# Optimization experiments

Hardware: AMD Instinct MI355X
Metric: run time of the kernel (lower is better)

## Reference

```python
import jax, jax.numpy as jnp
import numpy as np

EMBED_DIM = 1024
NUM_HEADS = 16
DIM_HEAD = EMBED_DIM // NUM_HEADS


def setup_inputs() -> dict:
    key = jax.random.key(0)
    ks = jax.random.split(key, 9)
    s = 1.0 / np.sqrt(EMBED_DIM)
    x = jax.random.normal(ks[0], (2, 2048, EMBED_DIM), dtype=jnp.float32)
    Wq = jax.random.uniform(ks[1], (EMBED_DIM, EMBED_DIM), jnp.float32, -s, s)
    bq = jax.random.uniform(ks[2], (EMBED_DIM,), jnp.float32, -s, s)
    Wk = jax.random.uniform(ks[3], (EMBED_DIM, EMBED_DIM), jnp.float32, -s, s)
    bk = jax.random.uniform(ks[4], (EMBED_DIM,), jnp.float32, -s, s)
    Wv = jax.random.uniform(ks[5], (EMBED_DIM, EMBED_DIM), jnp.float32, -s, s)
    bv = jax.random.uniform(ks[6], (EMBED_DIM,), jnp.float32, -s, s)
    Wo = jax.random.uniform(ks[7], (EMBED_DIM, EMBED_DIM), jnp.float32, -s, s)
    bo = jax.random.uniform(ks[8], (EMBED_DIM,), jnp.float32, -s, s)
    return {"x": x, "Wq": Wq, "bq": bq, "Wk": Wk, "bk": bk,
            "Wv": Wv, "bv": bv, "Wo": Wo, "bo": bo}


def reference(x, Wq, bq, Wk, bk, Wv, bv, Wo, bo):
    B, S, _ = x.shape
    # Linear layers (torch nn.Linear: x @ W.T + b), reshape to heads
    Q = (x @ Wq.T + bq).reshape(B, S, NUM_HEADS, DIM_HEAD)
    K = (x @ Wk.T + bk).reshape(B, S, NUM_HEADS, DIM_HEAD)
    V = (x @ Wv.T + bv).reshape(B, S, NUM_HEADS, DIM_HEAD)
    scores = jnp.einsum('bqhd,bkhd->bhqk', Q, K) / np.sqrt(DIM_HEAD)
    attn = jax.nn.softmax(scores, axis=-1)
    context = jnp.einsum('bhqk,bkhd->bqhd', attn, V).reshape(B, S, EMBED_DIM)
    return context @ Wo.T + bo
```

## Files before the change

### kernel.cpp

```cpp
#include <hip/hip_runtime.h>
#include <hip/hip_bf16.h>

#define SEQ   2048
#define EMB   1024
#define NHEAD 16
#define DHEAD 64
#define BATCH 2
#define MTOT  (BATCH*SEQ)
#define QT    64
#define KT    64

typedef __attribute__((ext_vector_type(8))) short s8v;
typedef __attribute__((ext_vector_type(4))) short s4v;
typedef __attribute__((ext_vector_type(4))) float f4v;

__device__ __forceinline__ short f2b(float f) {
    union { float fl; unsigned u; } v; v.fl = f;
    unsigned u = v.u;
    u = (u + 0x7fffu + ((u >> 16) & 1u)) >> 16;
    return (short)u;
}
__device__ __forceinline__ unsigned pk2(float a, float b) {
    union { __hip_bfloat162 h; unsigned u; } c;
    c.h = __float22bfloat162_rn(float2{a, b});
    return c.u;
}

#if __has_builtin(__builtin_amdgcn_exp2f)
__device__ __forceinline__ float exp2_fast(float x) { return __builtin_amdgcn_exp2f(x); }
#else
__device__ __forceinline__ float exp2_fast(float x) { return exp2f(x); }
#endif

__device__ __forceinline__ void pl32swap(unsigned &a, unsigned &b) {
    asm("v_permlane32_swap_b32 %0, %1" : "+v"(a), "+v"(b));
}
__device__ __forceinline__ void pl16swap(unsigned &a, unsigned &b) {
    asm("v_permlane16_swap_b32 %0, %1" : "+v"(a), "+v"(b));
}

__device__ __forceinline__ void bar_lds() {
    asm volatile("s_waitcnt lgkmcnt(0)\n\ts_barrier" ::: "memory");
}

__device__ __forceinline__ void gl_lds16(const short* g, short* l) {
    __builtin_amdgcn_global_load_lds(
        (const __attribute__((address_space(1))) void*)g,
        (__attribute__((address_space(3))) void*)l, 16, 0, 0);
}

__global__ __launch_bounds__(256)
void cvt_swz(const float* __restrict__ s0, const float* __restrict__ s1,
             const float* __restrict__ s2, const float* __restrict__ s3,
             const float* __restrict__ s4,
             short* __restrict__ d0, short* __restrict__ d1,
             short* __restrict__ d2, short* __restrict__ d3,
             short* __restrict__ d4)
{
    const int seg = blockIdx.y;
    const float* s = seg == 0 ? s0 : seg == 1 ? s1 : seg == 2 ? s2 : seg == 3 ? s3 : s4;
    short*       d = seg == 0 ? d0 : seg == 1 ? d1 : seg == 2 ? d2 : seg == 3 ? d3 : d4;
    const int nchunk = (seg == 0 ? MTOT * EMB : EMB * EMB) / 8;
    const int stride = gridDim.x * 256;
    for (int i = blockIdx.x * 256 + threadIdx.x; i < nchunk; i += stride) {
        const int row = i >> 7;
        const int c   = i & 127;
        const float4 v0 = *(const float4*)(s + (size_t)i * 8);
        const float4 v1 = *(const float4*)(s + (size_t)i * 8 + 4);
        s8v o;
        o[0] = f2b(v0.x); o[1] = f2b(v0.y); o[2] = f2b(v0.z); o[3] = f2b(v0.w);
        o[4] = f2b(v1.x); o[5] = f2b(v1.y); o[6] = f2b(v1.z); o[7] = f2b(v1.w);
        const int cp = (c & ~7) | ((c & 7) ^ (row & 7));
        *(s8v*)(d + (size_t)row * EMB + cp * 8) = o;
    }
}

template<int NT, bool FUSED3>
__global__ __launch_bounds__(256, 3)
void gemm_bb3(const short* __restrict__ A,
              const short* __restrict__ W0, const short* __restrict__ W1, const short* __restrict__ W2,
              const float* __restrict__ B0, const float* __restrict__ B1, const float* __restrict__ B2,
              void* __restrict__ C0, void* __restrict__ C1, void* __restrict__ C2)
{
    constexpr int JN = NT / 32;
    const int K = EMB, N = EMB;
    const int ntiles = EMB / NT;
    const int mat = blockIdx.x / ntiles;
    const int n0  = (blockIdx.x % ntiles) * NT;
    const int m0  = blockIdx.y * 128;
    const short* W  = (mat == 0) ? W0 : (mat == 1 ? W1 : W2);
    const float* Bi = (mat == 0) ? B0 : (mat == 1 ? B1 : B2);
    void*        C  = (mat == 0) ? C0 : (mat == 1 ? C1 : C2);
    const float qscale = (FUSED3 && mat == 0) ? 0.18033688f : 1.0f;

    __shared__ __align__(16) short As[128 * 64];
    __shared__ __align__(16) short Ws[NT * 64];

    const int tid  = threadIdx.x;
    const int lane = tid & 63;
    const int wave = tid >> 6;
    const int quad = lane >> 4;
    const int l16  = lane & 15;
    const int l8   = l16 & 7;
    const int wm   = wave >> 1;
    const int wn   = wave & 1;

    f4v acc[4][JN] = {};

    const int srow = lane >> 3;
    const int scol = (lane & 7) * 8;

    for (int k0 = 0; k0 < K; k0 += 64) {
        #pragma unroll
        for (int p = 0; p < 4; ++p) {
            const int rbase = wave * 32 + p * 8;
            gl_lds16(A + (size_t)(m0 + rbase + srow) * K + k0 + scol,
                     As + rbase * 64);
        }
        #pragma unroll
        for (int p = 0; p < NT / 32; ++p) {
            const int rbase = wave * (NT / 4) + p * 8;
            gl_lds16(W + (size_t)(n0 + rbase + srow) * K + k0 + scol,
                     Ws + rbase * 64);
        }
        __syncthreads();

        #pragma unroll
        for (int kk = 0; kk < 2; ++kk) {
            const int slot = ((kk * 4 + quad) ^ l8) * 8;
            s8v af[4], wf[JN];
            #pragma unroll
            for (int i = 0; i < 4; ++i)
                af[i] = *(const s8v*)(As + (wm * 64 + i * 16 + l16) * 64 + slot);
            #pragma unroll
            for (int j = 0; j < JN; ++j)
                wf[j] = *(const s8v*)(Ws + (wn * (NT / 2) + j * 16 + l16) * 64 + slot);
            #pragma unroll
            for (int i = 0; i < 4; ++i)
                #pragma unroll
                for (int j = 0; j < JN; ++j)
                    acc[i][j] = __builtin_amdgcn_mfma_f32_16x16x32_bf16(
                        af[i], wf[j], acc[i][j], 0, 0, 0);
        }
        __syncthreads();
    }

    #pragma unroll
    for (int j = 0; j < JN; ++j) {
        const int n = n0 + wn * (NT / 2) + j * 16 + l16;
        const float bv = Bi[n];
        #pragma unroll
        for (int i = 0; i < 4; ++i) {
            const int mb = m0 + wm * 64 + i * 16 + quad * 4;
            if (FUSED3 && mat == 2) {
                const int bb = mb >> 11, s = mb & 2047;
                s4v ov;
                #pragma unroll
                for (int rr = 0; rr < 4; ++rr) ov[rr] = f2b(acc[i][j][rr] + bv);
                *(s4v*)((short*)C + ((size_t)(bb * 1024 + n)) * SEQ + s) = ov;
            } else if (FUSED3) {
                #pragma unroll
                for (int rr = 0; rr < 4; ++rr)
                    ((short*)C)[(size_t)(mb + rr) * N + n] = f2b((acc[i][j][rr] + bv) * qscale);
            } else {
                #pragma unroll
                for (int rr = 0; rr < 4; ++rr)
                    ((float*)C)[(size_t)(mb + rr) * N + n] = acc[i][j][rr] + bv;
            }
        }
    }
}

__global__ __launch_bounds__(256, 4)
void attn_mfma6(const short* Q, const short* __restrict__ Kg,
                const short* __restrict__ Vt, short* O)
{
    const int i    = blockIdx.x;
    const int xcd  = i & 7;
    const int slot = i >> 3;
    const int combo = xcd * 4 + (slot >> 5);
    const int qb = slot & 31;
    const int h  = combo & 15;
    const int b  = combo >> 4;
    const int q0 = qb * QT;

    const int tid  = threadIdx.x;
    const int lane = tid & 63;
    const int wave = tid >> 6;
    const int quad = lane >> 4;
    const int l16  = lane & 15;
    const int l8   = l16 & 7;

    __shared__ __align__(16) short Ks[2][64 * 64];
    __shared__ __align__(16) short Vs[2][64 * 64];

    s8v qf[2];
    #pragma unroll
    for (int kk = 0; kk < 2; ++kk)
        qf[kk] = *(const s8v*)(Q + (size_t)(b * SEQ + q0 + wave * 16 + l16) * EMB
                                 + h * DHEAD + kk * 32 + quad * 8);

    f4v oacc[4] = {};
    f4v sacc    = {};
    s8v onef;
    #pragma unroll
    for (int e = 0; e < 8; ++e) onef[e] = (short)0x3F80;

    const int c = tid & 7, r = tid >> 3;
    const int swz = (c ^ (r & 7)) * 8;
    const size_t kbase = (size_t)(b * SEQ) * EMB + h * DHEAD;
    const size_t vbase = (size_t)((b * NHEAD + h) * DHEAD) * SEQ;

    s8v ka[2], va[2];
    #pragma unroll
    for (int p = 0; p < 2; ++p) {
        ka[p] = *(const s8v*)(Kg + kbase + (size_t)(r + p * 32) * EMB + c * 8);
        va[p] = *(const s8v*)(Vt + vbase + (size_t)(r + p * 32) * SEQ + c * 8);
    }

    for (int t = 0; t < SEQ / KT; ++t) {
        const int buf = t & 1;
        short* KsB = Ks[buf];
        short* VsB = Vs[buf];

        #pragma unroll
        for (int p = 0; p < 2; ++p) {
            *(s8v*)(KsB + (r + p * 32) * 64 + swz) = ka[p];
            *(s8v*)(VsB + (r + p * 32) * 64 + swz) = va[p];
        }
        if (t + 1 < SEQ / KT) {
            const int kt2 = (t + 1) * KT;
            #pragma unroll
            for (int p = 0; p < 2; ++p) {
                ka[p] = *(const s8v*)(Kg + kbase + (size_t)(kt2 + r + p * 32) * EMB + c * 8);
                va[p] = *(const s8v*)(Vt + vbase + (size_t)(r + p * 32) * SEQ + kt2 + c * 8);
            }
        }
        bar_lds();

        f4v sc[4] = {};
        #pragma unroll
        for (int kk = 0; kk < 2; ++kk) {
            const int ko = ((kk * 4 + quad) ^ l8) * 8;
            s8v kf[4];
            #pragma unroll
            for (int j = 0; j < 4; ++j)
                kf[j] = *(const s8v*)(KsB + (j * 16 + l16) * 64 + ko);
            #pragma unroll
            for (int j = 0; j < 4; ++j)
                sc[j] = __builtin_amdgcn_mfma_f32_16x16x32_bf16(
                    kf[j], qf[kk], sc[j], 0, 0, 0);
        }

        unsigned u[4][2];
        #pragma unroll
        for (int j = 0; j < 4; ++j) {
            u[j][0] = pk2(exp2_fast(sc[j][0]), exp2_fast(sc[j][1]));
            u[j][1] = pk2(exp2_fast(sc[j][2]), exp2_fast(sc[j][3]));
        }

        #pragma unroll
        for (int r2 = 0; r2 < 2; ++r2) {
            pl32swap(u[0][r2], u[1][r2]);
            pl32swap(u[2][r2], u[3][r2]);
            pl16swap(u[0][r2], u[1][r2]);
            pl16swap(u[2][r2], u[3][r2]);
        }
        union { unsigned uu[4]; s8v s; } pfa, pfb;
        pfa.uu[0] = u[0][0]; pfa.uu[1] = u[0][1]; pfa.uu[2] = u[1][0]; pfa.uu[3] = u[1][1];
        pfb.uu[0] = u[2][0]; pfb.uu[1] = u[2][1]; pfb.uu[2] = u[3][0]; pfb.uu[3] = u[3][1];

        #pragma unroll
        for (int kk = 0; kk < 2; ++kk) {
            const s8v pf = kk ? pfb.s : pfa.s;
            sacc = __builtin_amdgcn_mfma_f32_16x16x32_bf16(onef, pf, sacc, 0, 0, 0);
            const int ko = ((kk * 4 + quad) ^ l8) * 8;
            #pragma unroll
            for (int j = 0; j < 4; ++j) {
                const s8v vf = *(const s8v*)(VsB + (j * 16 + l16) * 64 + ko);
                oacc[j] = __builtin_amdgcn_mfma_f32_16x16x32_bf16(
                    vf, pf, oacc[j], 0, 0, 0);
            }
        }
    }

    const float inv = 1.0f / sacc[0];

    short* Os = (short*)Ks;
    #pragma unroll
    for (int j = 0; j < 4; ++j) {
        union { unsigned uu[2]; s4v s; } ov;
        ov.uu[0] = pk2(oacc[j][0] * inv, oacc[j][1] * inv);
        ov.uu[1] = pk2(oacc[j][2] * inv, oacc[j][3] * inv);
        const int pc = ((j * 2 + (quad >> 1)) ^ l8) * 8 + (quad & 1) * 4;
        *(s4v*)(Os + (wave * 16 + l16) * 64 + pc) = ov.s;
    }
    bar_lds();

    const int row = tid >> 2;
    const int cb  = (tid & 3) * 2;
    #pragma unroll
    for (int c4 = 0; c4 < 2; ++c4) {
        const int pcc = cb + c4;
        const s8v tt = *(const s8v*)(Os + row * 64 + pcc * 8);
        *(s8v*)(O + (size_t)(b * SEQ + q0 + row) * EMB + h * DHEAD + pcc * 8) = tt;
    }
}

extern "C" void kernel_launch(void* const* d_in, const int* in_sizes, int n_in,
                              void* d_out, int out_size, void* d_ws, size_t ws_size,
                              hipStream_t stream)
{
    const float* x  = (const float*)d_in[0];
    const float* Wq = (const float*)d_in[1];
    const float* bq = (const float*)d_in[2];
    const float* Wk = (const float*)d_in[3];
    const float* bk = (const float*)d_in[4];
    const float* Wv = (const float*)d_in[5];
    const float* bv = (const float*)d_in[6];
    const float* Wo = (const float*)d_in[7];
    const float* bo = (const float*)d_in[8];
    float* out = (float*)d_out;

    short* xb  = (short*)d_ws;
    short* Wqb = xb  + (size_t)MTOT * EMB;
    short* Wkb = Wqb + (size_t)EMB * EMB;
    short* Wvb = Wkb + (size_t)EMB * EMB;
    short* Wob = Wvb + (size_t)EMB * EMB;
    short* Qw  = Wob + (size_t)EMB * EMB;
    short* Kw  = Qw  + (size_t)MTOT * EMB;
    short* Vtw = Kw  + (size_t)MTOT * EMB;

    cvt_swz<<<dim3(512, 5), 256, 0, stream>>>(x, Wq, Wk, Wv, Wo,
                                              xb, Wqb, Wkb, Wvb, Wob);

    gemm_bb3<128, true><<<dim3(24, 32), 256, 0, stream>>>(
        xb, Wqb, Wkb, Wvb, bq, bk, bv, Qw, Kw, Vtw);

    attn_mfma6<<<dim3(BATCH * NHEAD * (SEQ / QT)), 256, 0, stream>>>(Qw, Kw, Vtw, Qw);

    gemm_bb3<64, false><<<dim3(16, 32), 256, 0, stream>>>(
        Qw, Wob, Wob, Wob, bo, bo, bo, out, out, out);
}
```

Before: 193.9 us.

## Double attention query tile and stream K/V straight into LDS

The attention kernel now processes 128 query rows per block with 512 threads instead of 64 rows with 256, so each K/V tile loaded into LDS is shared by twice as many query rows. K and V are copied with direct global-to-LDS loads: half the waves load K and half load V, double-buffered with one barrier per tile, replacing the register-staged copies. The aim is to halve K/V global traffic per query and remove register round-trips on the load path. In exchange the grid is half as large, which lowers parallelism, and the larger block raises register pressure per workgroup.

```diff
diff --git a/kernel.cpp b/kernel.cpp
--- a/kernel.cpp
+++ b/kernel.cpp
@@ -7,8 +7,9 @@
 #define DHEAD 64
 #define BATCH 2
 #define MTOT  (BATCH*SEQ)
-#define QT    64
+#define QT    128
 #define KT    64
+#define NTILE (SEQ/KT)
 
 typedef __attribute__((ext_vector_type(8))) short s8v;
 typedef __attribute__((ext_vector_type(4))) short s4v;
@@ -171,15 +172,15 @@
     }
 }
 
-__global__ __launch_bounds__(256, 4)
-void attn_mfma6(const short* Q, const short* __restrict__ Kg,
+__global__ __launch_bounds__(512, 4)
+void attn_mfma7(const short* Q, const short* __restrict__ Kg,
                 const short* __restrict__ Vt, short* O)
 {
     const int i    = blockIdx.x;
     const int xcd  = i & 7;
     const int slot = i >> 3;
-    const int combo = xcd * 4 + (slot >> 5);
-    const int qb = slot & 31;
+    const int combo = xcd * 4 + (slot >> 4);
+    const int qb = slot & 15;
     const int h  = combo & 15;
     const int b  = combo >> 4;
     const int q0 = qb * QT;
@@ -206,37 +207,33 @@
     #pragma unroll
     for (int e = 0; e < 8; ++e) onef[e] = (short)0x3F80;
 
-    const int c = tid & 7, r = tid >> 3;
-    const int swz = (c ^ (r & 7)) * 8;
+    const int r = lane >> 3, c = lane & 7;
+    const int sc8 = (c ^ r) * 8;
+    const bool isK = wave < 4;
+    const int wrow = (wave & 3) * 16;
     const size_t kbase = (size_t)(b * SEQ) * EMB + h * DHEAD;
     const size_t vbase = (size_t)((b * NHEAD + h) * DHEAD) * SEQ;
-
-    s8v ka[2], va[2];
-    #pragma unroll
-    for (int p = 0; p < 2; ++p) {
-        ka[p] = *(const s8v*)(Kg + kbase + (size_t)(r + p * 32) * EMB + c * 8);
-        va[p] = *(const s8v*)(Vt + vbase + (size_t)(r + p * 32) * SEQ + c * 8);
-    }
-
-    for (int t = 0; t < SEQ / KT; ++t) {
+    const short* gsrc = isK ? Kg + kbase + (size_t)(wrow + r) * EMB + sc8
+                            : Vt + vbase + (size_t)(wrow + r) * SEQ + sc8;
+    const size_t gstep8 = isK ? (size_t)8 * EMB : (size_t)8 * SEQ;
+    const size_t tstep  = isK ? (size_t)KT * EMB : (size_t)KT;
+    short* const lbase  = (isK ? (short*)Ks : (short*)Vs) + wrow * 64;
+
+    gl_lds16(gsrc,          lbase);
+    gl_lds16(gsrc + gstep8, lbase + 8 * 64);
+    const short* gnext = gsrc + tstep;
+
+    for (int t = 0; t < NTILE; ++t) {
         const int buf = t & 1;
-        short* KsB = Ks[buf];
-        short* VsB = Vs[buf];
-
-        #pragma unroll
-        for (int p = 0; p < 2; ++p) {
-            *(s8v*)(KsB + (r + p * 32) * 64 + swz) = ka[p];
-            *(s8v*)(VsB + (r + p * 32) * 64 + swz) = va[p];
-        }
-        if (t + 1 < SEQ / KT) {
-            const int kt2 = (t + 1) * KT;
-            #pragma unroll
-            for (int p = 0; p < 2; ++p) {
-                ka[p] = *(const s8v*)(Kg + kbase + (size_t)(kt2 + r + p * 32) * EMB + c * 8);
-                va[p] = *(const s8v*)(Vt + vbase + (size_t)(r + p * 32) * SEQ + kt2 + c * 8);
-            }
-        }
-        bar_lds();
+        __syncthreads();
+        if (t + 1 < NTILE) {
+            short* ldst = lbase + (buf ^ 1) * (64 * 64);
+            gl_lds16(gnext,          ldst);
+            gl_lds16(gnext + gstep8, ldst + 8 * 64);
+            gnext += tstep;
+        }
+        const short* KsB = Ks[buf];
+        const short* VsB = Vs[buf];
 
         f4v sc[4] = {};
         #pragma unroll
@@ -286,6 +283,7 @@
 
     const float inv = 1.0f / sacc[0];
 
+    __syncthreads();
     short* Os = (short*)Ks;
     #pragma unroll
     for (int j = 0; j < 4; ++j) {
@@ -337,7 +335,7 @@
     gemm_bb3<128, true><<<dim3(24, 32), 256, 0, stream>>>(
         xb, Wqb, Wkb, Wvb, bq, bk, bv, Qw, Kw, Vtw);
 
-    attn_mfma6<<<dim3(BATCH * NHEAD * (SEQ / QT)), 256, 0, stream>>>(Qw, Kw, Vtw, Qw);
+    attn_mfma7<<<dim3(BATCH * NHEAD * (SEQ / QT)), 512, 0, stream>>>(Qw, Kw, Vtw, Qw);
 
     gemm_bb3<64, false><<<dim3(16, 32), 256, 0, stream>>>(
         Qw, Wob, Wob, Wob, bo, bo, bo, out, out, out);
```

After: 185.3 us. 1.05x faster.
